# Kernel optimization log

Hardware: AMD Instinct MI355X
Metric: run time of the kernel (lower is better)

The kernel has to match this reference:

```python
import jax, jax.numpy as jnp
import numpy as np

N_ITER = 2
M = 0.0
AFF_SOFTMAX = 1.0
BIG = 1e16  # finite sentinel for invalid neighbors (CUDA kernel uses inf)


def _ssn(x, s):
    B, C, H, W = x.shape
    nh, nw = H // s, W // s
    S = nh * nw
    N = H * W
    # append_grid: concat (row, col) coordinate channels scaled by M/stoken
    ii, jj = jnp.meshgrid(jnp.arange(H), jnp.arange(W), indexing='ij')
    grid = jnp.stack([ii, jj], 0).astype(x.dtype) * (M / s)  # (2,H,W)
    xg = jnp.concatenate([x, jnp.broadcast_to(grid[None], (B, 2, H, W))], 1)
    C2 = C + 2
    # adaptive_avg_pool2d with exact divisibility == block mean
    cent = xg.reshape(B, C2, nh, s, nw, s).mean(axis=(3, 5)).reshape(B, C2, S)
    # nearest-neighbor init label map (exact divisibility => i//s)
    ly = jnp.broadcast_to((jnp.arange(H) // s)[:, None], (H, W)).reshape(-1)
    lx = jnp.broadcast_to((jnp.arange(W) // s)[None, :], (H, W)).reshape(-1)
    dy = jnp.repeat(jnp.arange(-1, 2), 3)  # 9-neighborhood offsets
    dx = jnp.tile(jnp.arange(-1, 2), 3)
    ny = ly[None, :] + dy[:, None]  # (9,N)
    nx = lx[None, :] + dx[:, None]
    valid = (ny >= 0) & (ny < nh) & (nx >= 0) & (nx < nw)
    nidx = jnp.clip(ny, 0, nh - 1) * nw + jnp.clip(nx, 0, nw - 1)  # (9,N)
    pix = jnp.arange(N)
    bidx = jnp.arange(B)[:, None, None]
    px = xg.reshape(B, C2, N)
    abs_aff = None
    for k in range(N_ITER):
        cg = cent[:, :, nidx]                              # (B,C2,9,N) gather
        dist = ((px[:, :, None, :] - cg) ** 2).sum(1)      # (B,9,N)
        dist = jnp.where(valid[None], dist, BIG)
        aff = jax.nn.softmax(-AFF_SOFTMAX * dist, axis=1)  # softmax over 9 nbrs
        aff = jnp.where(valid[None], aff, 0.0)
        # sparse_coo_tensor(...).to_dense() == scatter-add into (B,S,N)
        abs_aff = jnp.zeros((B, S, N), x.dtype).at[bidx, nidx[None], pix].add(aff)
        if k < N_ITER - 1:
            num = jnp.einsum('bsn,bcn->bcs', abs_aff, px)  # weighted bmm
            den = abs_aff.sum(2)[:, None] + 1e-16
            cent = num / den
    return abs_aff, S


def setup_inputs() -> dict:
    key = jax.random.key(0)
    x = jax.random.normal(key, (4, 32, 256, 256), dtype=jnp.float32)
    return {"x": x, "stoken_size": 16}


def reference(x, stoken_size):
    return _ssn(x, int(stoken_size))
```

## Files before the change

kernel.cpp:

```cpp
#include <hip/hip_runtime.h>
#include <hip/hip_fp16.h>

#define B_  4
#define C_  32
#define W_  256
#define N_  65536
#define NH_ 16
#define S_  256
#define PADP 260
#define PADH 260
#define PSTR 304

typedef float vf4 __attribute__((ext_vector_type(4)));
typedef _Float16 h4 __attribute__((ext_vector_type(4)));

__device__ __forceinline__ float wave_sum(float v) {
    v += __shfl_down(v, 32);
    v += __shfl_down(v, 16);
    v += __shfl_down(v, 8);
    v += __shfl_down(v, 4);
    v += __shfl_down(v, 2);
    v += __shfl_down(v, 1);
    return v;
}

__device__ __forceinline__ void st4(float* p, float a, float b, float c, float d) {
    vf4 v = {a, b, c, d};
    *(vf4*)p = v;
}

__device__ __forceinline__ void stage_tile(const float* __restrict__ x,
                                           int b, int sy, int sx, int t,
                                           float (*xsh)[PADP]) {
    const float* base = x + (size_t)b * C_ * N_ + (sy * 16) * W_ + sx * 16;
    #pragma unroll
    for (int i = 0; i < 8; ++i) {
        const int idx = i * 256 + t;
        const int c = idx >> 6, p4 = idx & 63;
        const float4 v = *(const float4*)(base + (size_t)c * N_ + (p4 >> 2) * W_ + (p4 & 3) * 4);
        *(float4*)&xsh[c][p4 * 4] = v;
    }
}

__device__ __forceinline__ void compute_aff(const float xv[C_], const float (*cl)[C_],
                                            int sy, int sx, float aff[9]) {
    float dist[9];
    #pragma unroll
    for (int k = 0; k < 9; ++k) {
        const int ny = sy + k / 3 - 1, nx = sx + k % 3 - 1;
        const bool valid = (ny >= 0) & (ny < NH_) & (nx >= 0) & (nx < NH_);
        float d = 0.f;
        #pragma unroll
        for (int c4 = 0; c4 < C_ / 4; ++c4) {
            const float4 cv = *(const float4*)&cl[k][c4 * 4];
            const float d0 = xv[c4 * 4 + 0] - cv.x;
            const float d1 = xv[c4 * 4 + 1] - cv.y;
            const float d2 = xv[c4 * 4 + 2] - cv.z;
            const float d3 = xv[c4 * 4 + 3] - cv.w;
            d += d0 * d0 + d1 * d1 + d2 * d2 + d3 * d3;
        }
        dist[k] = valid ? d : 1e30f;
    }
    float mind = dist[0];
    #pragma unroll
    for (int k = 1; k < 9; ++k) mind = fminf(mind, dist[k]);
    float sum = 0.f;
    #pragma unroll
    for (int k = 0; k < 9; ++k) {
        const float e = (dist[k] < 1e29f) ? __expf(mind - dist[k]) : 0.f;
        aff[k] = e;
        sum += e;
    }
    const float inv = 1.f / sum;
    #pragma unroll
    for (int k = 0; k < 9; ++k) aff[k] *= inv;
}

__device__ __forceinline__ float gather_cent1(const float* __restrict__ part,
                                              int b, int ny, int nx, int c) {
    float num = 0.f, den = 0.f;
    #pragma unroll
    for (int k2 = 0; k2 < 9; ++k2) {
        const int syp = ny - (k2 / 3 - 1), sxp = nx - (k2 % 3 - 1);
        if ((syp >= 0) & (syp < NH_) & (sxp >= 0) & (sxp < NH_)) {
            const size_t base = (size_t)(b * S_ + syp * NH_ + sxp) * PSTR;
            num += part[base + k2 * 32 + c];
            den += part[base + 288 + k2];
        }
    }
    return num / (den + 1e-16f);
}

__global__ __launch_bounds__(256) void k_cent0(const float* __restrict__ x,
                                               float* __restrict__ cent0) {
    const int blk = blockIdx.x;
    const int b = blk >> 8, s = blk & 255;
    const int sy = s >> 4, sx = s & 15;
    const int t = threadIdx.x;
    const int w = t >> 6, lane = t & 63;
    const float* base = x + (size_t)b * C_ * N_ + (sy * 16) * W_ + sx * 16;
    #pragma unroll
    for (int i = 0; i < 8; ++i) {
        const int c = i * 4 + w;
        const float4 v = *(const float4*)(base + (size_t)c * N_ + (lane >> 2) * W_ + (lane & 3) * 4);
        const float sm = wave_sum(v.x + v.y + v.z + v.w);
        if (lane == 0) cent0[(size_t)blk * C_ + c] = sm * (1.0f / 256.0f);
    }
}

__global__ __launch_bounds__(256, 4) void k_part(const float* __restrict__ x,
                                                 const float* __restrict__ cent0,
                                                 float* __restrict__ part) {
    const int blk = blockIdx.x;
    const int b = blk >> 8, s = blk & 255;
    const int sy = s >> 4, sx = s & 15;
    const int t = threadIdx.x;
    const int w = t >> 6, lane = t & 63;
    __shared__ float cl[9][C_];
    __shared__ float xsh[C_][PADP];
    __shared__ _Float16 affs[9][PADH];
    __shared__ float lden[4][9];
    {
        const int k = t >> 5, c = t & 31;
        const int ny = sy + k / 3 - 1, nx = sx + k % 3 - 1;
        const bool valid = (ny >= 0) & (ny < NH_) & (nx >= 0) & (nx < NH_);
        cl[k][c] = valid ? cent0[(size_t)(b * S_ + ny * NH_ + nx) * C_ + c] : 0.f;
    }
    if (t < 32) {
        const int ny = sy + 1, nx = sx + 1;
        const bool valid = (ny < NH_) & (nx < NH_);
        cl[8][t] = valid ? cent0[(size_t)(b * S_ + ny * NH_ + nx) * C_ + t] : 0.f;
    }
    stage_tile(x, b, sy, sx, t, xsh);
    __syncthreads();
    float xv[C_];
    #pragma unroll
    for (int c = 0; c < C_; ++c) xv[c] = xsh[c][t];
    float aff[9];
    compute_aff(xv, cl, sy, sx, aff);
    #pragma unroll
    for (int k = 0; k < 9; ++k) {
        affs[k][t] = (_Float16)aff[k];
        const float v = wave_sum(aff[k]);
        if (lane == 0) lden[w][k] = v;
    }
    __syncthreads();
    {
        const int k = t >> 5, c = t & 31;
        float acc = 0.f;
        #pragma unroll 4
        for (int p = 0; p < 256; p += 4) {
            const h4 a = *(const h4*)&affs[k][p];
            const float4 xc = *(const float4*)&xsh[c][p];
            acc += (float)a.x * xc.x + (float)a.y * xc.y +
                   (float)a.z * xc.z + (float)a.w * xc.w;
        }
        part[(size_t)blk * PSTR + t] = acc;
    }
    if (t < 32) {
        float acc = 0.f;
        #pragma unroll 4
        for (int p = 0; p < 256; p += 4) {
            const h4 a = *(const h4*)&affs[8][p];
            const float4 xc = *(const float4*)&xsh[t][p];
            acc += (float)a.x * xc.x + (float)a.y * xc.y +
                   (float)a.z * xc.z + (float)a.w * xc.w;
        }
        part[(size_t)blk * PSTR + 256 + t] = acc;
    }
    if (t < 9)
        part[(size_t)blk * PSTR + 288 + t] =
            lden[0][t] + lden[1][t] + lden[2][t] + lden[3][t];
}

__global__ __launch_bounds__(256, 4) void k_aff9(const float* __restrict__ x,
                                                 const float* __restrict__ part,
                                                 float* __restrict__ out) {
    const int blk = blockIdx.x;
    const int b = blk >> 8, s = blk & 255;
    const int sy = s >> 4, sx = s & 15;
    const int t = threadIdx.x;
    __shared__ float cl[9][C_];
    __shared__ float xsh[C_][PADP];
    __shared__ _Float16 affs[9][PADH];
    {
        const int k = t >> 5, c = t & 31;
        const int ny = sy + k / 3 - 1, nx = sx + k % 3 - 1;
        const bool valid = (ny >= 0) & (ny < NH_) & (nx >= 0) & (nx < NH_);
        cl[k][c] = valid ? gather_cent1(part, b, ny, nx, c) : 0.f;
    }
    if (t < 32) {
        const int ny = sy + 1, nx = sx + 1;
        const bool valid = (ny < NH_) & (nx < NH_);
        cl[8][t] = valid ? gather_cent1(part, b, ny, nx, t) : 0.f;
    }
    stage_tile(x, b, sy, sx, t, xsh);
    __syncthreads();
    float xv[C_];
    #pragma unroll
    for (int c = 0; c < C_; ++c) xv[c] = xsh[c][t];
    float aff[9];
    compute_aff(xv, cl, sy, sx, aff);
    #pragma unroll
    for (int k = 0; k < 9; ++k) affs[k][t] = (_Float16)aff[k];
    __syncthreads();
    #pragma unroll
    for (int i = 0; i < 3; ++i) {
        const int idx = i * 256 + t;
        if (idx < 576) {
            const int k = idx >> 6, j4 = idx & 63;
            const int ny = sy + k / 3 - 1, nx = sx + k % 3 - 1;
            if ((ny >= 0) & (ny < NH_) & (nx >= 0) & (nx < NH_)) {
                const h4 a = *(const h4*)&affs[k][j4 * 4];
                const int gq = (sy * 16 + (j4 >> 2)) * 64 + sx * 4 + (j4 & 3);
                float* dst = out + (((size_t)(b * S_ + ny * NH_ + nx) << 16) + gq * 4);
                st4(dst, (float)a.x, (float)a.y, (float)a.z, (float)a.w);
            }
        }
    }
    if ((blk | t) == 0) out[(size_t)B_ * S_ * N_] = 256.0f;
}

extern "C" void kernel_launch(void* const* d_in, const int* in_sizes, int n_in,
                              void* d_out, int out_size, void* d_ws, size_t ws_size,
                              hipStream_t stream) {
    const float* x = (const float*)d_in[0];
    float* ws = (float*)d_ws;
    float* cent0 = ws;
    float* part  = ws + 32768;
    float* out   = (float*)d_out;

    hipMemsetAsync(d_out, 0, (size_t)out_size * sizeof(float), stream);

    hipLaunchKernelGGL(k_cent0, dim3(B_ * S_), dim3(256), 0, stream, x, cent0);
    hipLaunchKernelGGL(k_part,  dim3(B_ * S_), dim3(256), 0, stream, x, cent0, part);
    hipLaunchKernelGGL(k_aff9,  dim3(B_ * S_), dim3(256), 0, stream, x, part, out);
}
```

Before: 341.6 us.

## Replace memset plus scatter with dense output-stationary write and tiled input layout

Removes the full-output memset and scattered affinity stores: affinities are first written compactly to a workspace, then a separate kernel writes every output element once, gathering nonzeros or writing zeros with coalesced vector stores. A new staging kernel transposes x into per-superpixel contiguous tiles and computes initial centroids in the same pass, so later kernels load tiles contiguously. This costs an extra transpose pass over the input and a workspace buffer for affinities.

```diff
diff --git a/kernel.cpp b/kernel.cpp
--- a/kernel.cpp
+++ b/kernel.cpp
@@ -8,11 +8,10 @@
 #define NH_ 16
 #define S_  256
 #define PADP 260
-#define PADH 260
 #define PSTR 304
+#define XT_TILE 8192
 
 typedef float vf4 __attribute__((ext_vector_type(4)));
-typedef _Float16 h4 __attribute__((ext_vector_type(4)));
 
 __device__ __forceinline__ float wave_sum(float v) {
     v += __shfl_down(v, 32);
@@ -24,20 +23,57 @@
     return v;
 }
 
-__device__ __forceinline__ void st4(float* p, float a, float b, float c, float d) {
-    vf4 v = {a, b, c, d};
-    *(vf4*)p = v;
-}
-
-__device__ __forceinline__ void stage_tile(const float* __restrict__ x,
-                                           int b, int sy, int sx, int t,
-                                           float (*xsh)[PADP]) {
-    const float* base = x + (size_t)b * C_ * N_ + (sy * 16) * W_ + sx * 16;
+__global__ __launch_bounds__(256) void k_stage(const float* __restrict__ x,
+                                               float* __restrict__ xt,
+                                               float* __restrict__ cent0) {
+    const int blk = blockIdx.x;
+    const int b = blk >> 8, c2 = (blk >> 4) & 15, sy = blk & 15;
+    const int t = threadIdx.x;
+    __shared__ float lds[2][16][260];
+    #pragma unroll
+    for (int i = 0; i < 8; ++i) {
+        const int idx = i * 256 + t;
+        const int c = idx >> 10, y = (idx >> 6) & 15, f = idx & 63;
+        const float4 v = *(const float4*)(
+            x + (((size_t)(b * 32 + c2 * 2 + c) * 256) + sy * 16 + y) * 256 + f * 4);
+        *(float4*)&lds[c][y][f * 4] = v;
+    }
+    __syncthreads();
+    const int w = t >> 6, lane = t & 63;
+    #pragma unroll
+    for (int j = 0; j < 8; ++j) {
+        const int chunk = w * 8 + j;
+        const int sx = chunk >> 1, c = chunk & 1;
+        const int py = lane >> 2, p4 = lane & 3;
+        const float4 v = *(const float4*)&lds[c][py][sx * 16 + p4 * 4];
+        const size_t tile = (size_t)(b * 256 + sy * 16 + sx);
+        *(float4*)(xt + tile * XT_TILE + (c2 * 2 + c) * 256 + py * 16 + p4 * 4) = v;
+    }
+    {
+        const int pair = t >> 3, sub = t & 7;
+        const int sx = pair >> 1, c = pair & 1;
+        float s = 0.f;
+        #pragma unroll
+        for (int i = 0; i < 32; ++i) {
+            const int px = sub * 32 + i;
+            s += lds[c][px >> 4][sx * 16 + (px & 15)];
+        }
+        s += __shfl_down(s, 4);
+        s += __shfl_down(s, 2);
+        s += __shfl_down(s, 1);
+        if (sub == 0)
+            cent0[(size_t)(b * 256 + sy * 16 + sx) * 32 + c2 * 2 + c] = s * (1.f / 256.f);
+    }
+}
+
+__device__ __forceinline__ void stage_tile_xt(const float* __restrict__ xt,
+                                              int blk, int t, float (*xsh)[PADP]) {
+    const float* base = xt + (size_t)blk * XT_TILE;
     #pragma unroll
     for (int i = 0; i < 8; ++i) {
         const int idx = i * 256 + t;
         const int c = idx >> 6, p4 = idx & 63;
-        const float4 v = *(const float4*)(base + (size_t)c * N_ + (p4 >> 2) * W_ + (p4 & 3) * 4);
+        const float4 v = *(const float4*)(base + (size_t)idx * 4);
         *(float4*)&xsh[c][p4 * 4] = v;
     }
 }
@@ -91,24 +127,11 @@
     return num / (den + 1e-16f);
 }
 
-__global__ __launch_bounds__(256) void k_cent0(const float* __restrict__ x,
-                                               float* __restrict__ cent0) {
-    const int blk = blockIdx.x;
-    const int b = blk >> 8, s = blk & 255;
-    const int sy = s >> 4, sx = s & 15;
-    const int t = threadIdx.x;
-    const int w = t >> 6, lane = t & 63;
-    const float* base = x + (size_t)b * C_ * N_ + (sy * 16) * W_ + sx * 16;
-    #pragma unroll
-    for (int i = 0; i < 8; ++i) {
-        const int c = i * 4 + w;
-        const float4 v = *(const float4*)(base + (size_t)c * N_ + (lane >> 2) * W_ + (lane & 3) * 4);
-        const float sm = wave_sum(v.x + v.y + v.z + v.w);
-        if (lane == 0) cent0[(size_t)blk * C_ + c] = sm * (1.0f / 256.0f);
-    }
-}
-
-__global__ __launch_bounds__(256, 4) void k_part(const float* __restrict__ x,
+typedef _Float16 h4_t;
+typedef _Float16 h4 __attribute__((ext_vector_type(4)));
+#define PADH 260
+
+__global__ __launch_bounds__(256, 4) void k_part(const float* __restrict__ xt,
                                                  const float* __restrict__ cent0,
                                                  float* __restrict__ part) {
     const int blk = blockIdx.x;
@@ -131,7 +154,7 @@
         const bool valid = (ny < NH_) & (nx < NH_);
         cl[8][t] = valid ? cent0[(size_t)(b * S_ + ny * NH_ + nx) * C_ + t] : 0.f;
     }
-    stage_tile(x, b, sy, sx, t, xsh);
+    stage_tile_xt(xt, blk, t, xsh);
     __syncthreads();
     float xv[C_];
     #pragma unroll
@@ -173,16 +196,15 @@
             lden[0][t] + lden[1][t] + lden[2][t] + lden[3][t];
 }
 
-__global__ __launch_bounds__(256, 4) void k_aff9(const float* __restrict__ x,
-                                                 const float* __restrict__ part,
-                                                 float* __restrict__ out) {
+__global__ __launch_bounds__(256, 4) void k_aff9v(const float* __restrict__ xt,
+                                                  const float* __restrict__ part,
+                                                  float* __restrict__ vals) {
     const int blk = blockIdx.x;
     const int b = blk >> 8, s = blk & 255;
     const int sy = s >> 4, sx = s & 15;
     const int t = threadIdx.x;
     __shared__ float cl[9][C_];
     __shared__ float xsh[C_][PADP];
-    __shared__ _Float16 affs[9][PADH];
     {
         const int k = t >> 5, c = t & 31;
         const int ny = sy + k / 3 - 1, nx = sx + k % 3 - 1;
@@ -194,7 +216,7 @@
         const bool valid = (ny < NH_) & (nx < NH_);
         cl[8][t] = valid ? gather_cent1(part, b, ny, nx, t) : 0.f;
     }
-    stage_tile(x, b, sy, sx, t, xsh);
+    stage_tile_xt(xt, blk, t, xsh);
     __syncthreads();
     float xv[C_];
     #pragma unroll
@@ -202,23 +224,34 @@
     float aff[9];
     compute_aff(xv, cl, sy, sx, aff);
     #pragma unroll
-    for (int k = 0; k < 9; ++k) affs[k][t] = (_Float16)aff[k];
-    __syncthreads();
-    #pragma unroll
-    for (int i = 0; i < 3; ++i) {
-        const int idx = i * 256 + t;
-        if (idx < 576) {
-            const int k = idx >> 6, j4 = idx & 63;
-            const int ny = sy + k / 3 - 1, nx = sx + k % 3 - 1;
-            if ((ny >= 0) & (ny < NH_) & (nx >= 0) & (nx < NH_)) {
-                const h4 a = *(const h4*)&affs[k][j4 * 4];
-                const int gq = (sy * 16 + (j4 >> 2)) * 64 + sx * 4 + (j4 & 3);
-                float* dst = out + (((size_t)(b * S_ + ny * NH_ + nx) << 16) + gq * 4);
-                st4(dst, (float)a.x, (float)a.y, (float)a.z, (float)a.w);
-            }
-        }
-    }
-    if ((blk | t) == 0) out[(size_t)B_ * S_ * N_] = 256.0f;
+    for (int k = 0; k < 9; ++k)
+        vals[(((size_t)blk * 9) + k) * 256 + t] = aff[k];
+}
+
+__global__ __launch_bounds__(256) void k_write(const float* __restrict__ vals,
+                                               float* __restrict__ out) {
+    const size_t tid = (size_t)blockIdx.x * 256 + threadIdx.x;
+    vf4* po = (vf4*)out;
+    #pragma unroll 4
+    for (int i = 0; i < 32; ++i) {
+        const size_t q = tid + (size_t)i * 524288;
+        const int b   = (int)(q >> 22);
+        const int r   = (int)(q & 4194303);
+        const int sp  = r >> 14;
+        const int n4  = r & 16383;
+        const int py  = n4 >> 6, px4 = n4 & 63;
+        const int syp = sp >> 4,  sxp = sp & 15;
+        const int ty  = py >> 4,  tx  = px4 >> 2;
+        vf4 v = {0.f, 0.f, 0.f, 0.f};
+        if (((unsigned)(ty - syp + 1) <= 2u) & ((unsigned)(tx - sxp + 1) <= 2u)) {
+            const int ssrc = ty * 16 + tx;
+            const int kp   = (syp - ty + 1) * 3 + (sxp - tx + 1);
+            const int pl   = (py & 15) * 16 + (px4 & 3) * 4;
+            v = *(const vf4*)&vals[(((size_t)(b * S_ + ssrc) * 9) + kp) * 256 + pl];
+        }
+        po[q] = v;
+    }
+    if (tid == 0) out[(size_t)B_ * S_ * N_] = 256.0f;
 }
 
 extern "C" void kernel_launch(void* const* d_in, const int* in_sizes, int n_in,
@@ -226,13 +259,14 @@
                               hipStream_t stream) {
     const float* x = (const float*)d_in[0];
     float* ws = (float*)d_ws;
-    float* cent0 = ws;
-    float* part  = ws + 32768;
+    float* xt    = ws;
+    float* cent0 = ws + 8388608;
+    float* part  = ws + 8388608 + 32768;
+    float* vals  = ws + 8388608 + 32768 + 311296;
     float* out   = (float*)d_out;
 
-    hipMemsetAsync(d_out, 0, (size_t)out_size * sizeof(float), stream);
-
-    hipLaunchKernelGGL(k_cent0, dim3(B_ * S_), dim3(256), 0, stream, x, cent0);
-    hipLaunchKernelGGL(k_part,  dim3(B_ * S_), dim3(256), 0, stream, x, cent0, part);
-    hipLaunchKernelGGL(k_aff9,  dim3(B_ * S_), dim3(256), 0, stream, x, part, out);
-}
+    hipLaunchKernelGGL(k_stage, dim3(1024),    dim3(256), 0, stream, x, xt, cent0);
+    hipLaunchKernelGGL(k_part,  dim3(B_ * S_), dim3(256), 0, stream, xt, cent0, part);
+    hipLaunchKernelGGL(k_aff9v, dim3(B_ * S_), dim3(256), 0, stream, xt, part, vals);
+    hipLaunchKernelGGL(k_write, dim3(2048),    dim3(256), 0, stream, vals, out);
+}
```

New measurement: 338.1 us. No clear change (-1.0%).
